# Kernel tuning notes

Hardware: AMD Instinct MI355X
Metric: run time of the kernel (lower is better)

The kernel has to match this reference:

```python
import jax, jax.numpy as jnp
import numpy as np

N_ATOMS = 4_000_000   # number of atoms (batched over the per-atom Python loop)
N_PARTS = 1024        # number of molecular parts (size of atom_charge table)
D = 16                # fixed feature width from Linear(16,16)


def setup_inputs() -> dict:
    key = jax.random.key(0)
    ks = jax.random.split(key, 9)
    atom_type_vector = jax.random.normal(ks[0], (N_ATOMS, D), dtype=jnp.float32)
    atom_charge = jax.random.normal(ks[1], (N_PARTS,), dtype=jnp.float32)
    # three Linear(16,16) layers, PyTorch layout: y = x @ W.T + b
    W1 = jax.random.normal(ks[2], (D, D), dtype=jnp.float32) * 0.25
    b1 = jax.random.normal(ks[3], (D,), dtype=jnp.float32) * 0.1
    W2 = jax.random.normal(ks[4], (D, D), dtype=jnp.float32) * 0.25
    b2 = jax.random.normal(ks[5], (D,), dtype=jnp.float32) * 0.1
    W3 = jax.random.normal(ks[6], (D, D), dtype=jnp.float32) * 0.25
    b3 = jax.random.normal(ks[7], (D,), dtype=jnp.float32) * 0.1
    atom_part = jax.random.randint(ks[8], (N_ATOMS,), 0, N_PARTS, dtype=jnp.int64)
    return {"atom_type_vector": atom_type_vector, "atom_charge": atom_charge,
            "W1": W1, "b1": b1, "W2": W2, "b2": b2, "W3": W3, "b3": b3,
            "atom_part": atom_part}


def reference(atom_type_vector, atom_charge, W1, b1, W2, b2, W3, b3, atom_part):
    # Batched version of the per-atom loop:
    # nodes[i] = MLP(atom_type_vector[i]) + atom_part[i] + atom_charge[atom_part[i]]
    h = jax.nn.elu(atom_type_vector @ W1.T + b1)
    h = jax.nn.elu(h @ W2.T + b2)
    h = jax.nn.elu(h @ W3.T + b3)          # [N, 16]
    add = atom_part.astype(h.dtype) + atom_charge[atom_part]  # [N] broadcast scalars
    return h + add[:, None]
```

## Files before the change

kernel.cpp:

```cpp
#include <hip/hip_runtime.h>
#include <math.h>

#define D 16
#define NPARTS 1024
#define BLOCK 256

__global__ __launch_bounds__(BLOCK, 4) void nodes_mlp_kernel(
    const float* __restrict__ x,
    const float* __restrict__ charge,
    const float* __restrict__ W1, const float* __restrict__ b1,
    const float* __restrict__ W2, const float* __restrict__ b2,
    const float* __restrict__ W3, const float* __restrict__ b3,
    const int*   __restrict__ part,
    float* __restrict__ out,
    int n)
{
    __shared__ float sq[NPARTS];
    const int t = threadIdx.x;
    for (int i = t; i < NPARTS; i += BLOCK) sq[i] = charge[i];
    __syncthreads();

    const long long idx = (long long)blockIdx.x * BLOCK + t;
    if (idx >= (long long)n) return;

    const int prt = part[idx];

    const float4* xp = (const float4*)(x + idx * D);
    float4 v0 = xp[0], v1 = xp[1], v2 = xp[2], v3 = xp[3];

    float h[D];
    h[0]  = v0.x; h[1]  = v0.y; h[2]  = v0.z; h[3]  = v0.w;
    h[4]  = v1.x; h[5]  = v1.y; h[6]  = v1.z; h[7]  = v1.w;
    h[8]  = v2.x; h[9]  = v2.y; h[10] = v2.z; h[11] = v2.w;
    h[12] = v3.x; h[13] = v3.y; h[14] = v3.z; h[15] = v3.w;

    const float* Ws[3] = {W1, W2, W3};
    const float* bs[3] = {b1, b2, b3};

#pragma unroll
    for (int L = 0; L < 3; ++L) {
        const float* __restrict__ W = Ws[L];
        const float* __restrict__ b = bs[L];
        float o[D];
#pragma unroll
        for (int j = 0; j < D; ++j) {
            float acc = b[j];
#pragma unroll
            for (int k = 0; k < D; ++k) {
                acc += h[k] * W[j * D + k];
            }
            o[j] = acc;
        }
#pragma unroll
        for (int j = 0; j < D; ++j) {
            float v = o[j];
            h[j] = (v > 0.0f) ? v : (__expf(v) - 1.0f);
        }
    }

    const float add = (float)prt + sq[prt];

    float4 r0 = make_float4(h[0]  + add, h[1]  + add, h[2]  + add, h[3]  + add);
    float4 r1 = make_float4(h[4]  + add, h[5]  + add, h[6]  + add, h[7]  + add);
    float4 r2 = make_float4(h[8]  + add, h[9]  + add, h[10] + add, h[11] + add);
    float4 r3 = make_float4(h[12] + add, h[13] + add, h[14] + add, h[15] + add);

    float4* op = (float4*)(out + idx * D);
    op[0] = r0; op[1] = r1; op[2] = r2; op[3] = r3;
}

extern "C" void kernel_launch(void* const* d_in, const int* in_sizes, int n_in,
                              void* d_out, int out_size, void* d_ws, size_t ws_size,
                              hipStream_t stream) {
    const float* x      = (const float*)d_in[0];
    const float* charge = (const float*)d_in[1];
    const float* W1     = (const float*)d_in[2];
    const float* b1     = (const float*)d_in[3];
    const float* W2     = (const float*)d_in[4];
    const float* b2     = (const float*)d_in[5];
    const float* W3     = (const float*)d_in[6];
    const float* b3     = (const float*)d_in[7];
    const int*   part   = (const int*)d_in[8];
    float* out = (float*)d_out;

    const int n = in_sizes[8];
    const int grid = (n + BLOCK - 1) / BLOCK;

    nodes_mlp_kernel<<<grid, BLOCK, 0, stream>>>(
        x, charge, W1, b1, W2, b2, W3, b3, part, out, n);
}
```

Measured before the change: 510.2 us.

## Run the three-layer MLP on fp16 MFMA tiles with a persistent grid

Replaces the per-thread scalar 16x16 FMA loops with one 16x16x16 fp16 MFMA per layer. Each wave handles a tile of 16 atoms, and weights and biases stay in registers. The grid becomes persistent and grid-strides over tiles, which removes the scalar FMA compute cost and the per-block charge-table reload. The trade-off is fp16 rounding of the inputs and intermediate activations, which may exceed the accuracy tolerance.

```diff
diff --git a/kernel.cpp b/kernel.cpp
--- a/kernel.cpp
+++ b/kernel.cpp
@@ -1,11 +1,15 @@
 #include <hip/hip_runtime.h>
 #include <math.h>
 
-#define D 16
 #define NPARTS 1024
 #define BLOCK 256
+#define WPB (BLOCK / 64)
+#define GRID_BLOCKS 2048
 
-__global__ __launch_bounds__(BLOCK, 4) void nodes_mlp_kernel(
+typedef __attribute__((ext_vector_type(4))) _Float16 half4;
+typedef __attribute__((ext_vector_type(4))) float floatx4;
+
+__global__ __launch_bounds__(BLOCK, 8) void nodes_mlp_mfma(
     const float* __restrict__ x,
     const float* __restrict__ charge,
     const float* __restrict__ W1, const float* __restrict__ b1,
@@ -16,57 +20,82 @@
     int n)
 {
     __shared__ float sq[NPARTS];
-    const int t = threadIdx.x;
-    for (int i = t; i < NPARTS; i += BLOCK) sq[i] = charge[i];
+    for (int i = threadIdx.x; i < NPARTS; i += BLOCK) sq[i] = charge[i];
     __syncthreads();
 
-    const long long idx = (long long)blockIdx.x * BLOCK + t;
-    if (idx >= (long long)n) return;
+    const int lane = threadIdx.x & 63;
+    const int col  = lane & 15;
+    const int g    = lane >> 4;
 
-    const int prt = part[idx];
-
-    const float4* xp = (const float4*)(x + idx * D);
-    float4 v0 = xp[0], v1 = xp[1], v2 = xp[2], v3 = xp[3];
-
-    float h[D];
-    h[0]  = v0.x; h[1]  = v0.y; h[2]  = v0.z; h[3]  = v0.w;
-    h[4]  = v1.x; h[5]  = v1.y; h[6]  = v1.z; h[7]  = v1.w;
-    h[8]  = v2.x; h[9]  = v2.y; h[10] = v2.z; h[11] = v2.w;
-    h[12] = v3.x; h[13] = v3.y; h[14] = v3.z; h[15] = v3.w;
-
-    const float* Ws[3] = {W1, W2, W3};
-    const float* bs[3] = {b1, b2, b3};
-
+    half4  aW[3];
+    floatx4 cB[3];
+    {
+        const float* Ws[3] = {W1, W2, W3};
+        const float* bs[3] = {b1, b2, b3};
 #pragma unroll
-    for (int L = 0; L < 3; ++L) {
-        const float* __restrict__ W = Ws[L];
-        const float* __restrict__ b = bs[L];
-        float o[D];
-#pragma unroll
-        for (int j = 0; j < D; ++j) {
-            float acc = b[j];
-#pragma unroll
-            for (int k = 0; k < D; ++k) {
-                acc += h[k] * W[j * D + k];
-            }
-            o[j] = acc;
-        }
-#pragma unroll
-        for (int j = 0; j < D; ++j) {
-            float v = o[j];
-            h[j] = (v > 0.0f) ? v : (__expf(v) - 1.0f);
+        for (int L = 0; L < 3; ++L) {
+            const float4 wv = *(const float4*)(Ws[L] + col * 16 + 4 * g);
+            half4 a;
+            a[0] = (_Float16)wv.x; a[1] = (_Float16)wv.y;
+            a[2] = (_Float16)wv.z; a[3] = (_Float16)wv.w;
+            aW[L] = a;
+            const float4 bv = *(const float4*)(bs[L] + 4 * g);
+            floatx4 c;
+            c[0] = bv.x; c[1] = bv.y; c[2] = bv.z; c[3] = bv.w;
+            cB[L] = c;
         }
     }
 
-    const float add = (float)prt + sq[prt];
+    const int ntiles = (n + 15) >> 4;
+    const int nwaves = gridDim.x * WPB;
 
-    float4 r0 = make_float4(h[0]  + add, h[1]  + add, h[2]  + add, h[3]  + add);
-    float4 r1 = make_float4(h[4]  + add, h[5]  + add, h[6]  + add, h[7]  + add);
-    float4 r2 = make_float4(h[8]  + add, h[9]  + add, h[10] + add, h[11] + add);
-    float4 r3 = make_float4(h[12] + add, h[13] + add, h[14] + add, h[15] + add);
+    for (int tile = blockIdx.x * WPB + (threadIdx.x >> 6);
+         tile < ntiles; tile += nwaves) {
 
-    float4* op = (float4*)(out + idx * D);
-    op[0] = r0; op[1] = r1; op[2] = r2; op[3] = r3;
+        const int row  = tile * 16 + col;
+        const int rowc = (row < n) ? row : (n - 1);
+
+        const float4 xv = *(const float4*)(x + rowc * 16 + 4 * g);
+        half4 bx;
+        bx[0] = (_Float16)xv.x; bx[1] = (_Float16)xv.y;
+        bx[2] = (_Float16)xv.z; bx[3] = (_Float16)xv.w;
+
+        floatx4 d = __builtin_amdgcn_mfma_f32_16x16x16f16(aW[0], bx, cB[0], 0, 0, 0);
+
+        half4 h2;
+#pragma unroll
+        for (int i = 0; i < 4; ++i) {
+            float v = d[i];
+            v = (v > 0.0f) ? v : (__expf(v) - 1.0f);
+            h2[i] = (_Float16)v;
+        }
+        d = __builtin_amdgcn_mfma_f32_16x16x16f16(aW[1], h2, cB[1], 0, 0, 0);
+
+        half4 h3;
+#pragma unroll
+        for (int i = 0; i < 4; ++i) {
+            float v = d[i];
+            v = (v > 0.0f) ? v : (__expf(v) - 1.0f);
+            h3[i] = (_Float16)v;
+        }
+        d = __builtin_amdgcn_mfma_f32_16x16x16f16(aW[2], h3, cB[2], 0, 0, 0);
+
+        const int   p   = part[rowc];
+        const float add = (float)p + sq[p];
+
+        float4 r;
+        {
+            float v0 = d[0]; v0 = (v0 > 0.0f) ? v0 : (__expf(v0) - 1.0f);
+            float v1 = d[1]; v1 = (v1 > 0.0f) ? v1 : (__expf(v1) - 1.0f);
+            float v2 = d[2]; v2 = (v2 > 0.0f) ? v2 : (__expf(v2) - 1.0f);
+            float v3 = d[3]; v3 = (v3 > 0.0f) ? v3 : (__expf(v3) - 1.0f);
+            r = make_float4(v0 + add, v1 + add, v2 + add, v3 + add);
+        }
+
+        if (row < n) {
+            *(float4*)(out + row * 16 + 4 * g) = r;
+        }
+    }
 }
 
 extern "C" void kernel_launch(void* const* d_in, const int* in_sizes, int n_in,
@@ -83,9 +112,11 @@
     const int*   part   = (const int*)d_in[8];
     float* out = (float*)d_out;
 
-    const int n = in_sizes[8];
-    const int grid = (n + BLOCK - 1) / BLOCK;
+    const int n      = in_sizes[8];
+    const int ntiles = (n + 15) >> 4;
+    int grid = (ntiles + WPB - 1) / WPB;
+    if (grid > GRID_BLOCKS) grid = GRID_BLOCKS;
 
-    nodes_mlp_kernel<<<grid, BLOCK, 0, stream>>>(
+    nodes_mlp_mfma<<<grid, BLOCK, 0, stream>>>(
         x, charge, W1, b1, W2, b2, W3, b3, part, out, n);
 }
```

New measurement: 436.9 us. -14.4%, faster.
